# Performance work log

Hardware: AMD Instinct MI355X
Metric: run time of the kernel (lower is better)

## Reference

```python
import jax, jax.numpy as jnp
import numpy as np

N, NFEAT, NHID = 10000, 128, 64


def _gc(x, adj, W, b):
    # GraphConvolution: adj @ (x @ W) + b
    return adj @ (x @ W) + b


def _fwd(x, adj, Wg0, bg0, Wg1, bg1, Wt0, bt0, Wt1, bt1,
         W000, b000, W001, b001, W100, b100, W101, b101,
         Wo0, bo0, Wo1, bo1, Wpp, bpp, Wpp2, bpp2, a, t):
    H = Wg0.shape[1]
    # outcome GCN stack (n_in=2), dropout is eval no-op
    rep_o = jax.nn.relu(_gc(x, adj, Wg0, bg0))
    rep_o = jax.nn.relu(_gc(rep_o, adj, Wg1, bg1))
    # treatment GCN stack
    rep_t = jax.nn.relu(_gc(x, adj, Wt0, bt0))
    rep_t = jax.nn.relu(_gc(rep_t, adj, Wt1, bt1))

    rep_cat = jnp.concatenate([rep_o, rep_t], axis=1)  # [N, 2H]
    # edge score(i,j) = [rep_cat_i ; rep_cat_j] @ a  =  s_src_i + s_dst_j
    s_src = rep_cat @ a[:2 * H, 0]   # [N]
    s_dst = rep_cat @ a[2 * H:, 0]   # [N]
    scores = s_src[:, None] + s_dst[None, :]          # [N, N]
    # only nonzero adj entries get a score; rest remain 0 (index_put into zeros)
    att = jnp.where(adj != 0, scores, jnp.zeros((), scores.dtype))
    att = jax.nn.softmax(att, axis=1)                 # full dense row softmax

    rep_out = att @ rep_t + rep_o                     # [N, H]

    treatment = jax.nn.sigmoid((rep_t @ Wpp + bpp) @ Wpp2 + bpp2)  # [N, 2]

    rep0 = rep_out
    rep1 = rep_out
    y00 = jax.nn.relu(rep0 @ W000 + b000)
    y10 = jax.nn.relu(rep1 @ W100 + b100)
    y00 = jax.nn.relu(y00 @ W001 + b001)
    y10 = jax.nn.relu(y10 @ W101 + b101)
    y0 = (y00 @ Wo0 + bo0).reshape(-1)
    y1 = (y10 @ Wo1 + bo1).reshape(-1)
    y = jnp.where(t > 0, y1, y0)
    return (y, rep_out, treatment)


def setup_inputs() -> dict:
    key = jax.random.key(0)
    ks = jax.random.split(key, 32)
    H = NHID
    x = jax.random.normal(ks[0], (N, NFEAT), dtype=jnp.float32)
    u = jax.random.uniform(ks[1], (N, N), dtype=jnp.float32)
    adj = jnp.where(u < 0.002, u, jnp.zeros((), jnp.float32))
    t = jax.random.randint(ks[2], (N,), 0, 2, dtype=jnp.int32)

    def lin(k, fi, fo):
        s = 1.0 / np.sqrt(fi)
        kw, kb = jax.random.split(k)
        return (jax.random.uniform(kw, (fi, fo), jnp.float32, -s, s),
                jax.random.uniform(kb, (fo,), jnp.float32, -s, s))

    Wg0, bg0 = lin(ks[3], NFEAT, H)
    Wg1, bg1 = lin(ks[4], H, H)
    Wt0, bt0 = lin(ks[5], NFEAT, H)
    Wt1, bt1 = lin(ks[6], H, H)
    W000, b000 = lin(ks[7], H, H)
    W001, b001 = lin(ks[8], H, H)
    W100, b100 = lin(ks[9], H, H)
    W101, b101 = lin(ks[10], H, H)
    Wo0, bo0 = lin(ks[11], H, 1)
    Wo1, bo1 = lin(ks[12], H, 1)
    Wpp, bpp = lin(ks[13], H, H)
    Wpp2, bpp2 = lin(ks[14], H, 2)
    # torch init is xavier with gain=0 (all zeros); use small random for a
    # meaningful correctness baseline
    a = jax.random.normal(ks[15], (4 * H, 1), dtype=jnp.float32) * 0.1
    return dict(x=x, adj=adj, t=t,
                Wg0=Wg0, bg0=bg0, Wg1=Wg1, bg1=bg1,
                Wt0=Wt0, bt0=bt0, Wt1=Wt1, bt1=bt1,
                W000=W000, b000=b000, W001=W001, b001=b001,
                W100=W100, b100=b100, W101=W101, b101=b101,
                Wo0=Wo0, bo0=bo0, Wo1=Wo1, bo1=bo1,
                Wpp=Wpp, bpp=bpp, Wpp2=Wpp2, bpp2=bpp2, a=a)


def reference(x, adj, t, Wg0, bg0, Wg1, bg1, Wt0, bt0, Wt1, bt1,
              W000, b000, W001, b001, W100, b100, W101, b101,
              Wo0, bo0, Wo1, bo1, Wpp, bpp, Wpp2, bpp2, a):
    return _fwd(x, adj, Wg0, bg0, Wg1, bg1, Wt0, bt0, Wt1, bt1,
                W000, b000, W001, b001, W100, b100, W101, b101,
                Wo0, bo0, Wo1, bo1, Wpp, bpp, Wpp2, bpp2, a, t)
```

## Files before the change

### kernel.cpp

```cpp
#include <hip/hip_runtime.h>
#include <hip/hip_bf16.h>

#define N_NODES 10000
#define ROW4    2500
#define CAP     64
#define GEMM_BLOCKS 1250

#define OFF_CNT     0
#define OFF_COLSUM  10000
#define OFF_COLS    10064
#define OFF_VALS    650064
#define OFF_SSRC    1290064
#define OFF_SDST    1300064
#define OFF_B1      1310064
#define OFF_B2      1950064
#define OFF_B3      2590064
#define OFF_B4      3230064

__device__ __forceinline__ float wave_sum(float v) {
    #pragma unroll
    for (int off = 32; off >= 1; off >>= 1) v += __shfl_xor(v, off, 64);
    return v;
}
__device__ __forceinline__ float wave_max(float v) {
    #pragma unroll
    for (int off = 32; off >= 1; off >>= 1) v = fmaxf(v, __shfl_xor(v, off, 64));
    return v;
}

__global__ void k1_fused(const float4* __restrict__ adj4, const float* __restrict__ x,
                         const float* __restrict__ Wg0, const float* __restrict__ Wt0,
                         int* __restrict__ cnt, int* __restrict__ cols,
                         float* __restrict__ vals, float* __restrict__ colsum,
                         float* __restrict__ P, float* __restrict__ Q) {
    __shared__ float xs[8 * 128];
    int tid = threadIdx.x;
    if (blockIdx.x < GEMM_BLOCKS) {
        int row0 = blockIdx.x * 8;
        ((float4*)xs)[tid] = ((const float4*)(x + (size_t)row0 * 128))[tid];
        if (blockIdx.x == 0 && tid < 64) colsum[tid] = 0.0f;
        __syncthreads();
        int sub = tid >> 6, f = tid & 63;
        #pragma unroll
        for (int g = 0; g < 2; ++g) {
            const float* xr = xs + (g * 4 + sub) * 128;
            float aP = 0.0f, aQ = 0.0f;
            #pragma unroll 8
            for (int k = 0; k < 128; k += 4) {
                float4 xv = *(const float4*)(xr + k);
                aP += xv.x * Wg0[(k + 0) * 64 + f] + xv.y * Wg0[(k + 1) * 64 + f]
                    + xv.z * Wg0[(k + 2) * 64 + f] + xv.w * Wg0[(k + 3) * 64 + f];
                aQ += xv.x * Wt0[(k + 0) * 64 + f] + xv.y * Wt0[(k + 1) * 64 + f]
                    + xv.z * Wt0[(k + 2) * 64 + f] + xv.w * Wt0[(k + 3) * 64 + f];
            }
            P[(size_t)(row0 + g * 4 + sub) * 64 + f] = aP;
            Q[(size_t)(row0 + g * 4 + sub) * 64 + f] = aQ;
        }
    } else {
        int lane = tid & 63, w = tid >> 6;
        int row = (blockIdx.x - GEMM_BLOCKS) * 4 + w;
        const float4* rp = adj4 + (size_t)row * ROW4;
        size_t base = (size_t)row * CAP;
        int count = 0;
        for (int it = 0; it < 40; ++it) {
            int idx = it * 64 + lane;
            float4 v = make_float4(0.f, 0.f, 0.f, 0.f);
            if (idx < ROW4) v = rp[idx];
            float vv[4] = {v.x, v.y, v.z, v.w};
            bool any = (v.x != 0.f) | (v.y != 0.f) | (v.z != 0.f) | (v.w != 0.f);
            if (__ballot(any)) {
                #pragma unroll
                for (int l = 0; l < 4; ++l) {
                    unsigned long long b = __ballot(vv[l] != 0.f);
                    if (b) {
                        int pre = __popcll(b & ((1ull << lane) - 1ull));
                        if (vv[l] != 0.f) {
                            int pos = count + pre;
                            if (pos < CAP) {
                                cols[base + pos] = idx * 4 + l;
                                vals[base + pos] = vv[l];
                            }
                        }
                        count += (int)__popcll(b);
                    }
                }
            }
        }
        if (lane == 0) cnt[row] = min(count, CAP);
    }
}

__global__ void k2_agg_gemm(const int* __restrict__ cnt, const int* __restrict__ cols,
                            const float* __restrict__ vals,
                            const float* __restrict__ P, const float* __restrict__ Q,
                            const float* __restrict__ bg0, const float* __restrict__ bt0,
                            const float* __restrict__ Wg1, const float* __restrict__ Wt1,
                            float* __restrict__ P2, float* __restrict__ Q2) {
    __shared__ float ra[8 * 64], rb[8 * 64];
    int tid = threadIdx.x, row0 = blockIdx.x * 8, sub = tid >> 6, f = tid & 63;
    float bo = bg0[f], bt = bt0[f];
    #pragma unroll
    for (int g = 0; g < 2; ++g) {
        int lr = g * 4 + sub, row = row0 + lr;
        int c = min(cnt[row], CAP);
        float v_l = 0.0f; int c_l = 0;
        if (f < c) { c_l = cols[(size_t)row * CAP + f]; v_l = vals[(size_t)row * CAP + f]; }
        float a0 = 0.f, a1 = 0.f, b0 = 0.f, b1 = 0.f;
        for (int p = 0; p < c; p += 8) {
            #pragma unroll
            for (int j = 0; j < 8; j += 2) {
                float vv0 = __shfl(v_l, p + j, 64);     int cc0 = __shfl(c_l, p + j, 64);
                float vv1 = __shfl(v_l, p + j + 1, 64); int cc1 = __shfl(c_l, p + j + 1, 64);
                a0 += vv0 * P[(size_t)cc0 * 64 + f];
                b0 += vv0 * Q[(size_t)cc0 * 64 + f];
                a1 += vv1 * P[(size_t)cc1 * 64 + f];
                b1 += vv1 * Q[(size_t)cc1 * 64 + f];
            }
        }
        ra[lr * 64 + f] = fmaxf(a0 + a1 + bo, 0.0f);
        rb[lr * 64 + f] = fmaxf(b0 + b1 + bt, 0.0f);
    }
    __syncthreads();
    #pragma unroll
    for (int g = 0; g < 2; ++g) {
        int lr = g * 4 + sub, row = row0 + lr;
        const float* rra = ra + lr * 64;
        const float* rrb = rb + lr * 64;
        float aA = 0.f, aB = 0.f;
        #pragma unroll 8
        for (int k = 0; k < 64; k += 4) {
            float4 va = *(const float4*)(rra + k);
            float4 vb = *(const float4*)(rrb + k);
            aA += va.x * Wg1[(k + 0) * 64 + f] + va.y * Wg1[(k + 1) * 64 + f]
                + va.z * Wg1[(k + 2) * 64 + f] + va.w * Wg1[(k + 3) * 64 + f];
            aB += vb.x * Wt1[(k + 0) * 64 + f] + vb.y * Wt1[(k + 1) * 64 + f]
                + vb.z * Wt1[(k + 2) * 64 + f] + vb.w * Wt1[(k + 3) * 64 + f];
        }
        P2[(size_t)row * 64 + f] = aA;
        Q2[(size_t)row * 64 + f] = aB;
    }
}

__global__ void k3_agg_score(const int* __restrict__ cnt, const int* __restrict__ cols,
                             const float* __restrict__ vals,
                             const float* __restrict__ P2, const float* __restrict__ Q2,
                             const float* __restrict__ bg1, const float* __restrict__ bt1,
                             const float* __restrict__ a,
                             const float* __restrict__ Wpp, const float* __restrict__ bpp,
                             const float* __restrict__ Wpp2, const float* __restrict__ bpp2,
                             float* __restrict__ rep_o, float* __restrict__ rep_t,
                             float* __restrict__ s_src, float* __restrict__ s_dst,
                             float* __restrict__ colsum, float* __restrict__ out_trt) {
    __shared__ float rts[8 * 64];
    int tid = threadIdx.x, row0 = blockIdx.x * 8, sub = tid >> 6, f = tid & 63;
    float bo = bg1[f], bt = bt1[f];
    float a0c = a[f], a1c = a[64 + f], a2c = a[128 + f], a3c = a[192 + f];
    #pragma unroll
    for (int g = 0; g < 2; ++g) {
        int lr = g * 4 + sub, row = row0 + lr;
        int c = min(cnt[row], CAP);
        float v_l = 0.0f; int c_l = 0;
        if (f < c) { c_l = cols[(size_t)row * CAP + f]; v_l = vals[(size_t)row * CAP + f]; }
        float a0 = 0.f, a1 = 0.f, b0 = 0.f, b1 = 0.f;
        for (int p = 0; p < c; p += 8) {
            #pragma unroll
            for (int j = 0; j < 8; j += 2) {
                float vv0 = __shfl(v_l, p + j, 64);     int cc0 = __shfl(c_l, p + j, 64);
                float vv1 = __shfl(v_l, p + j + 1, 64); int cc1 = __shfl(c_l, p + j + 1, 64);
                a0 += vv0 * P2[(size_t)cc0 * 64 + f];
                b0 += vv0 * Q2[(size_t)cc0 * 64 + f];
                a1 += vv1 * P2[(size_t)cc1 * 64 + f];
                b1 += vv1 * Q2[(size_t)cc1 * 64 + f];
            }
        }
        float vo = fmaxf(a0 + a1 + bo, 0.0f);
        float vt = fmaxf(b0 + b1 + bt, 0.0f);
        rep_o[(size_t)row * 64 + f] = vo;
        rep_t[(size_t)row * 64 + f] = vt;
        rts[lr * 64 + f] = vt;
        float ps = wave_sum(vo * a0c + vt * a1c);
        float pd = wave_sum(vo * a2c + vt * a3c);
        if (f == 0) { s_src[row] = ps; s_dst[row] = pd; }
    }
    __syncthreads();
    if (sub == 0) {
        float cs = 0.0f;
        #pragma unroll
        for (int lr = 0; lr < 8; ++lr) cs += rts[lr * 64 + f];
        atomicAdd(&colsum[f], cs);
    }
    float bp = bpp[f], w20 = Wpp2[f * 2 + 0], w21 = Wpp2[f * 2 + 1];
    #pragma unroll
    for (int g = 0; g < 2; ++g) {
        int lr = g * 4 + sub, row = row0 + lr;
        const float* rr = rts + lr * 64;
        float u = bp;
        #pragma unroll 8
        for (int k = 0; k < 64; k += 4) {
            float4 rv = *(const float4*)(rr + k);
            u += rv.x * Wpp[(k + 0) * 64 + f] + rv.y * Wpp[(k + 1) * 64 + f]
               + rv.z * Wpp[(k + 2) * 64 + f] + rv.w * Wpp[(k + 3) * 64 + f];
        }
        float p0 = wave_sum(u * w20);
        float p1 = wave_sum(u * w21);
        if (f == 0) {
            out_trt[(size_t)row * 2 + 0] = 1.0f / (1.0f + expf(-(p0 + bpp2[0])));
            out_trt[(size_t)row * 2 + 1] = 1.0f / (1.0f + expf(-(p1 + bpp2[1])));
        }
    }
}

__global__ void k4_attn_heads(const int* __restrict__ cnt, const int* __restrict__ cols,
                              const float* __restrict__ s_src, const float* __restrict__ s_dst,
                              const float* __restrict__ colsum,
                              const float* __restrict__ rep_o, const float* __restrict__ rep_t,
                              const float* __restrict__ W000, const float* __restrict__ b000,
                              const float* __restrict__ W001, const float* __restrict__ b001,
                              const float* __restrict__ W100, const float* __restrict__ b100,
                              const float* __restrict__ W101, const float* __restrict__ b101,
                              const float* __restrict__ Wo0, const float* __restrict__ bo0,
                              const float* __restrict__ Wo1, const float* __restrict__ bo1,
                              const int* __restrict__ t,
                              float* __restrict__ out_y, float* __restrict__ out_rep) {
    __shared__ float reps[8 * 64], u0s[8 * 64], u1s[8 * 64];
    int tid = threadIdx.x, row0 = blockIdx.x * 8, sub = tid >> 6, f = tid & 63;
    float csf = colsum[f];
    #pragma unroll
    for (int g = 0; g < 2; ++g) {
        int lr = g * 4 + sub, row = row0 + lr;
        int c = min(cnt[row], CAP);
        float ssrc = s_src[row];
        int   col_l = (f < c) ? cols[(size_t)row * CAP + f] : 0;
        float s_l   = (f < c) ? ssrc + s_dst[col_l] : -1e30f;
        float m = fmaxf(wave_max(s_l), 0.0f);
        float e_l = (f < c) ? expf(s_l - m) : 0.0f;
        float em = expf(-m);
        float Z = wave_sum(e_l) + (float)(N_NODES - c) * em;
        float g_l = (f < c) ? (e_l - em) : 0.0f;
        float a0 = 0.f, a1 = 0.f, a2 = 0.f, a3 = 0.f;
        for (int p = 0; p < c; p += 8) {
            #pragma unroll
            for (int j = 0; j < 8; j += 4) {
                float g0 = __shfl(g_l, p + j + 0, 64); int c0 = __shfl(col_l, p + j + 0, 64);
                float g1 = __shfl(g_l, p + j + 1, 64); int c1 = __shfl(col_l, p + j + 1, 64);
                float g2 = __shfl(g_l, p + j + 2, 64); int c2 = __shfl(col_l, p + j + 2, 64);
                float g3 = __shfl(g_l, p + j + 3, 64); int c3 = __shfl(col_l, p + j + 3, 64);
                a0 += g0 * rep_t[(size_t)c0 * 64 + f];
                a1 += g1 * rep_t[(size_t)c1 * 64 + f];
                a2 += g2 * rep_t[(size_t)c2 * 64 + f];
                a3 += g3 * rep_t[(size_t)c3 * 64 + f];
            }
        }
        float outv = ((a0 + a1 + a2 + a3) + em * csf) / Z + rep_o[(size_t)row * 64 + f];
        out_rep[(size_t)row * 64 + f] = outv;
        reps[lr * 64 + f] = outv;
    }
    __syncthreads();
    float bA = b000[f], bB = b100[f];
    #pragma unroll
    for (int g = 0; g < 2; ++g) {
        int lr = g * 4 + sub;
        const float* rr = reps + lr * 64;
        float u0 = bA, u1 = bB;
        #pragma unroll 8
        for (int k = 0; k < 64; k += 4) {
            float4 rv = *(const float4*)(rr + k);
            u0 += rv.x * W000[(k + 0) * 64 + f] + rv.y * W000[(k + 1) * 64 + f]
                + rv.z * W000[(k + 2) * 64 + f] + rv.w * W000[(k + 3) * 64 + f];
            u1 += rv.x * W100[(k + 0) * 64 + f] + rv.y * W100[(k + 1) * 64 + f]
                + rv.z * W100[(k + 2) * 64 + f] + rv.w * W100[(k + 3) * 64 + f];
        }
        u0s[lr * 64 + f] = fmaxf(u0, 0.0f);
        u1s[lr * 64 + f] = fmaxf(u1, 0.0f);
    }
    __syncthreads();
    float bC = b001[f], bD = b101[f], wo0 = Wo0[f], wo1 = Wo1[f];
    #pragma unroll
    for (int g = 0; g < 2; ++g) {
        int lr = g * 4 + sub, row = row0 + lr;
        const float* r0 = u0s + lr * 64;
        const float* r1 = u1s + lr * 64;
        float v0 = bC, v1 = bD;
        #pragma unroll 8
        for (int k = 0; k < 64; k += 4) {
            float4 q0 = *(const float4*)(r0 + k);
            float4 q1 = *(const float4*)(r1 + k);
            v0 += q0.x * W001[(k + 0) * 64 + f] + q0.y * W001[(k + 1) * 64 + f]
                + q0.z * W001[(k + 2) * 64 + f] + q0.w * W001[(k + 3) * 64 + f];
            v1 += q1.x * W101[(k + 0) * 64 + f] + q1.y * W101[(k + 1) * 64 + f]
                + q1.z * W101[(k + 2) * 64 + f] + q1.w * W101[(k + 3) * 64 + f];
        }
        float y0 = wave_sum(fmaxf(v0, 0.0f) * wo0);
        float y1 = wave_sum(fmaxf(v1, 0.0f) * wo1);
        if (f == 0)
            out_y[row] = (t[row] > 0) ? (y1 + bo1[0]) : (y0 + bo0[0]);
    }
}


extern "C" void kernel_launch(void* const* d_in, const int* in_sizes, int n_in,
                              void* d_out, int out_size, void* d_ws, size_t ws_size,
                              hipStream_t stream) {
    const float* x    = (const float*)d_in[0];
    const float* adj  = (const float*)d_in[1];
    const int*   t    = (const int*)d_in[2];
    const float* Wg0  = (const float*)d_in[3];
    const float* bg0  = (const float*)d_in[4];
    const float* Wg1  = (const float*)d_in[5];
    const float* bg1  = (const float*)d_in[6];
    const float* Wt0  = (const float*)d_in[7];
    const float* bt0  = (const float*)d_in[8];
    const float* Wt1  = (const float*)d_in[9];
    const float* bt1  = (const float*)d_in[10];
    const float* W000 = (const float*)d_in[11];
    const float* b000 = (const float*)d_in[12];
    const float* W001 = (const float*)d_in[13];
    const float* b001 = (const float*)d_in[14];
    const float* W100 = (const float*)d_in[15];
    const float* b100 = (const float*)d_in[16];
    const float* W101 = (const float*)d_in[17];
    const float* b101 = (const float*)d_in[18];
    const float* Wo0  = (const float*)d_in[19];
    const float* bo0  = (const float*)d_in[20];
    const float* Wo1  = (const float*)d_in[21];
    const float* bo1  = (const float*)d_in[22];
    const float* Wpp  = (const float*)d_in[23];
    const float* bpp  = (const float*)d_in[24];
    const float* Wpp2 = (const float*)d_in[25];
    const float* bpp2 = (const float*)d_in[26];
    const float* a    = (const float*)d_in[27];

    float* ws = (float*)d_ws;
    int*   cnt    = (int*)(ws + OFF_CNT);
    float* colsum = ws + OFF_COLSUM;
    int*   cols   = (int*)(ws + OFF_COLS);
    float* vals   = ws + OFF_VALS;
    float* s_src  = ws + OFF_SSRC;
    float* s_dst  = ws + OFF_SDST;
    float* B1     = ws + OFF_B1;
    float* B2     = ws + OFF_B2;
    float* B3     = ws + OFF_B3;
    float* B4     = ws + OFF_B4;

    float* out_y   = (float*)d_out;
    float* out_rep = (float*)d_out + N_NODES;
    float* out_trt = (float*)d_out + N_NODES + N_NODES * 64;

    k1_fused<<<GEMM_BLOCKS + 2500, 256, 0, stream>>>((const float4*)adj, x, Wg0, Wt0,
                                                     cnt, cols, vals, colsum, B1, B2);
    k2_agg_gemm<<<1250, 256, 0, stream>>>(cnt, cols, vals, B1, B2, bg0, bt0, Wg1, Wt1, B3, B4);
    k3_agg_score<<<1250, 256, 0, stream>>>(cnt, cols, vals, B3, B4, bg1, bt1, a,
                                           Wpp, bpp, Wpp2, bpp2,
                                           B1, B2, s_src, s_dst, colsum, out_trt);
    k4_attn_heads<<<1250, 256, 0, stream>>>(cnt, cols, s_src, s_dst, colsum, B1, B2,
                                            W000, b000, W001, b001,
                                            W100, b100, W101, b101,
                                            Wo0, bo0, Wo1, bo1, t, out_y, out_rep);
}
```

Baseline: 690.4 us.

## Merge four kernels into one cooperative persistent kernel with grid syncs

Replaces the four separate kernel launches with a single cooperative persistent kernel whose blocks loop over row chunks and separate the phases with grid-wide syncs. It also packs column indices and values into interleaved float2 pairs so each neighbour needs one load instead of two. The aim is to cut launch overhead and the gaps between dependent kernels. In exchange it caps the grid size, adds grid-sync cost, and calls an occupancy query on the host for every launch.

```diff
diff --git a/kernel.cpp b/kernel.cpp
--- a/kernel.cpp
+++ b/kernel.cpp
@@ -1,17 +1,22 @@
 #include <hip/hip_runtime.h>
-#include <hip/hip_bf16.h>
+#include <hip/hip_cooperative_groups.h>
+
+namespace cg = cooperative_groups;
 
 #define N_NODES 10000
 #define ROW4    2500
 #define CAP     64
-#define GEMM_BLOCKS 1250
+#define GEMM_CHUNKS 1250
+#define SPAR_CHUNKS 2500
+#define TOTAL_A     (GEMM_CHUNKS + SPAR_CHUNKS)
+#define ROW_CHUNKS  1250
+#define MAX_GRID    1024
 
 #define OFF_CNT     0
 #define OFF_COLSUM  10000
-#define OFF_COLS    10064
-#define OFF_VALS    650064
-#define OFF_SSRC    1290064
-#define OFF_SDST    1300064
+#define OFF_SSRC    10064
+#define OFF_SDST    20064
+#define OFF_PAIRS   30064
 #define OFF_B1      1310064
 #define OFF_B2      1950064
 #define OFF_B3      2590064
@@ -28,332 +33,315 @@
     return v;
 }
 
-__global__ void k1_fused(const float4* __restrict__ adj4, const float* __restrict__ x,
-                         const float* __restrict__ Wg0, const float* __restrict__ Wt0,
-                         int* __restrict__ cnt, int* __restrict__ cols,
-                         float* __restrict__ vals, float* __restrict__ colsum,
-                         float* __restrict__ P, float* __restrict__ Q) {
-    __shared__ float xs[8 * 128];
-    int tid = threadIdx.x;
-    if (blockIdx.x < GEMM_BLOCKS) {
-        int row0 = blockIdx.x * 8;
-        ((float4*)xs)[tid] = ((const float4*)(x + (size_t)row0 * 128))[tid];
-        if (blockIdx.x == 0 && tid < 64) colsum[tid] = 0.0f;
-        __syncthreads();
-        int sub = tid >> 6, f = tid & 63;
-        #pragma unroll
-        for (int g = 0; g < 2; ++g) {
-            const float* xr = xs + (g * 4 + sub) * 128;
-            float aP = 0.0f, aQ = 0.0f;
-            #pragma unroll 8
-            for (int k = 0; k < 128; k += 4) {
-                float4 xv = *(const float4*)(xr + k);
-                aP += xv.x * Wg0[(k + 0) * 64 + f] + xv.y * Wg0[(k + 1) * 64 + f]
-                    + xv.z * Wg0[(k + 2) * 64 + f] + xv.w * Wg0[(k + 3) * 64 + f];
-                aQ += xv.x * Wt0[(k + 0) * 64 + f] + xv.y * Wt0[(k + 1) * 64 + f]
-                    + xv.z * Wt0[(k + 2) * 64 + f] + xv.w * Wt0[(k + 3) * 64 + f];
-            }
-            P[(size_t)(row0 + g * 4 + sub) * 64 + f] = aP;
-            Q[(size_t)(row0 + g * 4 + sub) * 64 + f] = aQ;
+struct KArgs {
+    const float4* adj4; const float* x; const int* t;
+    const float *Wg0, *bg0, *Wg1, *bg1, *Wt0, *bt0, *Wt1, *bt1;
+    const float *W000, *b000, *W001, *b001, *W100, *b100, *W101, *b101;
+    const float *Wo0, *bo0, *Wo1, *bo1, *Wpp, *bpp, *Wpp2, *bpp2, *a;
+    int* cnt; float2* pairs;
+    float *colsum, *s_src, *s_dst, *B1, *B2, *B3, *B4;
+    float *out_y, *out_rep, *out_trt;
+};
+
+__global__ __launch_bounds__(256, 4) void mega(KArgs A) {
+    __shared__ float smem[1536];
+    const int tid = threadIdx.x;
+    const int sub = tid >> 6, f = tid & 63;
+    cg::grid_group grid = cg::this_grid();
+
+    if (blockIdx.x == 0 && tid < 64) A.colsum[tid] = 0.0f;
+    for (int chunk = blockIdx.x; chunk < TOTAL_A; chunk += gridDim.x) {
+        if (chunk < GEMM_CHUNKS) {
+            int row0 = chunk * 8;
+            float* xs = smem;
+            ((float4*)xs)[tid] = ((const float4*)(A.x + (size_t)row0 * 128))[tid];
+            __syncthreads();
+            #pragma unroll
+            for (int g = 0; g < 2; ++g) {
+                const float* xr = xs + (g * 4 + sub) * 128;
+                float aP = 0.0f, aQ = 0.0f;
+                #pragma unroll 8
+                for (int k = 0; k < 128; k += 4) {
+                    float4 xv = *(const float4*)(xr + k);
+                    aP += xv.x * A.Wg0[(k + 0) * 64 + f] + xv.y * A.Wg0[(k + 1) * 64 + f]
+                        + xv.z * A.Wg0[(k + 2) * 64 + f] + xv.w * A.Wg0[(k + 3) * 64 + f];
+                    aQ += xv.x * A.Wt0[(k + 0) * 64 + f] + xv.y * A.Wt0[(k + 1) * 64 + f]
+                        + xv.z * A.Wt0[(k + 2) * 64 + f] + xv.w * A.Wt0[(k + 3) * 64 + f];
+                }
+                A.B1[(size_t)(row0 + g * 4 + sub) * 64 + f] = aP;
+                A.B2[(size_t)(row0 + g * 4 + sub) * 64 + f] = aQ;
+            }
+            __syncthreads();
+        } else {
+            int row = (chunk - GEMM_CHUNKS) * 4 + sub;
+            const float4* rp = A.adj4 + (size_t)row * ROW4;
+            size_t base = (size_t)row * CAP;
+            int count = 0;
+            for (int it = 0; it < 40; ++it) {
+                int idx = it * 64 + f;
+                float4 v = make_float4(0.f, 0.f, 0.f, 0.f);
+                if (idx < ROW4) v = rp[idx];
+                float vv[4] = {v.x, v.y, v.z, v.w};
+                bool any = (v.x != 0.f) | (v.y != 0.f) | (v.z != 0.f) | (v.w != 0.f);
+                if (__ballot(any)) {
+                    #pragma unroll
+                    for (int l = 0; l < 4; ++l) {
+                        unsigned long long b = __ballot(vv[l] != 0.f);
+                        if (b) {
+                            int pre = __popcll(b & ((1ull << f) - 1ull));
+                            if (vv[l] != 0.f) {
+                                int pos = count + pre;
+                                if (pos < CAP)
+                                    A.pairs[base + pos] =
+                                        make_float2(__int_as_float(idx * 4 + l), vv[l]);
+                            }
+                            count += (int)__popcll(b);
+                        }
+                    }
+                }
+            }
+            if (f == 0) A.cnt[row] = min(count, CAP);
         }
-    } else {
-        int lane = tid & 63, w = tid >> 6;
-        int row = (blockIdx.x - GEMM_BLOCKS) * 4 + w;
-        const float4* rp = adj4 + (size_t)row * ROW4;
-        size_t base = (size_t)row * CAP;
-        int count = 0;
-        for (int it = 0; it < 40; ++it) {
-            int idx = it * 64 + lane;
-            float4 v = make_float4(0.f, 0.f, 0.f, 0.f);
-            if (idx < ROW4) v = rp[idx];
-            float vv[4] = {v.x, v.y, v.z, v.w};
-            bool any = (v.x != 0.f) | (v.y != 0.f) | (v.z != 0.f) | (v.w != 0.f);
-            if (__ballot(any)) {
+    }
+    grid.sync();
+
+    {
+        float* ra = smem; float* rb = smem + 512;
+        float bo = A.bg0[f], bt = A.bt0[f];
+        for (int chunk = blockIdx.x; chunk < ROW_CHUNKS; chunk += gridDim.x) {
+            int row0 = chunk * 8;
+            #pragma unroll
+            for (int g = 0; g < 2; ++g) {
+                int lr = g * 4 + sub, row = row0 + lr;
+                int c = min(A.cnt[row], CAP);
+                float2 pr = make_float2(0.f, 0.f);
+                if (f < c) pr = A.pairs[(size_t)row * CAP + f];
+                int c_l = __float_as_int(pr.x); float v_l = pr.y;
+                float a0 = 0.f, a1 = 0.f, b0 = 0.f, b1 = 0.f;
+                for (int p = 0; p < c; p += 8) {
+                    #pragma unroll
+                    for (int j = 0; j < 8; j += 2) {
+                        float vv0 = __shfl(v_l, p + j, 64);     int cc0 = __shfl(c_l, p + j, 64);
+                        float vv1 = __shfl(v_l, p + j + 1, 64); int cc1 = __shfl(c_l, p + j + 1, 64);
+                        a0 += vv0 * A.B1[(size_t)cc0 * 64 + f];
+                        b0 += vv0 * A.B2[(size_t)cc0 * 64 + f];
+                        a1 += vv1 * A.B1[(size_t)cc1 * 64 + f];
+                        b1 += vv1 * A.B2[(size_t)cc1 * 64 + f];
+                    }
+                }
+                ra[lr * 64 + f] = fmaxf(a0 + a1 + bo, 0.0f);
+                rb[lr * 64 + f] = fmaxf(b0 + b1 + bt, 0.0f);
+            }
+            __syncthreads();
+            #pragma unroll
+            for (int g = 0; g < 2; ++g) {
+                int lr = g * 4 + sub, row = row0 + lr;
+                const float* rra = ra + lr * 64;
+                const float* rrb = rb + lr * 64;
+                float aA = 0.f, aB = 0.f;
+                #pragma unroll 8
+                for (int k = 0; k < 64; k += 4) {
+                    float4 va = *(const float4*)(rra + k);
+                    float4 vb = *(const float4*)(rrb + k);
+                    aA += va.x * A.Wg1[(k + 0) * 64 + f] + va.y * A.Wg1[(k + 1) * 64 + f]
+                        + va.z * A.Wg1[(k + 2) * 64 + f] + va.w * A.Wg1[(k + 3) * 64 + f];
+                    aB += vb.x * A.Wt1[(k + 0) * 64 + f] + vb.y * A.Wt1[(k + 1) * 64 + f]
+                        + vb.z * A.Wt1[(k + 2) * 64 + f] + vb.w * A.Wt1[(k + 3) * 64 + f];
+                }
+                A.B3[(size_t)row * 64 + f] = aA;
+                A.B4[(size_t)row * 64 + f] = aB;
+            }
+            __syncthreads();
+        }
+    }
+    grid.sync();
+
+    {
+        float* rts = smem;
+        float bo = A.bg1[f], bt = A.bt1[f];
+        float a0c = A.a[f], a1c = A.a[64 + f], a2c = A.a[128 + f], a3c = A.a[192 + f];
+        float bp = A.bpp[f], w20 = A.Wpp2[f * 2 + 0], w21 = A.Wpp2[f * 2 + 1];
+        for (int chunk = blockIdx.x; chunk < ROW_CHUNKS; chunk += gridDim.x) {
+            int row0 = chunk * 8;
+            #pragma unroll
+            for (int g = 0; g < 2; ++g) {
+                int lr = g * 4 + sub, row = row0 + lr;
+                int c = min(A.cnt[row], CAP);
+                float2 pr = make_float2(0.f, 0.f);
+                if (f < c) pr = A.pairs[(size_t)row * CAP + f];
+                int c_l = __float_as_int(pr.x); float v_l = pr.y;
+                float a0 = 0.f, a1 = 0.f, b0 = 0.f, b1 = 0.f;
+                for (int p = 0; p < c; p += 8) {
+                    #pragma unroll
+                    for (int j = 0; j < 8; j += 2) {
+                        float vv0 = __shfl(v_l, p + j, 64);     int cc0 = __shfl(c_l, p + j, 64);
+                        float vv1 = __shfl(v_l, p + j + 1, 64); int cc1 = __shfl(c_l, p + j + 1, 64);
+                        a0 += vv0 * A.B3[(size_t)cc0 * 64 + f];
+                        b0 += vv0 * A.B4[(size_t)cc0 * 64 + f];
+                        a1 += vv1 * A.B3[(size_t)cc1 * 64 + f];
+                        b1 += vv1 * A.B4[(size_t)cc1 * 64 + f];
+                    }
+                }
+                float vo = fmaxf(a0 + a1 + bo, 0.0f);
+                float vt = fmaxf(b0 + b1 + bt, 0.0f);
+                A.B1[(size_t)row * 64 + f] = vo;
+                A.B2[(size_t)row * 64 + f] = vt;
+                rts[lr * 64 + f] = vt;
+                float ps = wave_sum(vo * a0c + vt * a1c);
+                float pd = wave_sum(vo * a2c + vt * a3c);
+                if (f == 0) { A.s_src[row] = ps; A.s_dst[row] = pd; }
+            }
+            __syncthreads();
+            if (sub == 0) {
+                float cs = 0.0f;
                 #pragma unroll
-                for (int l = 0; l < 4; ++l) {
-                    unsigned long long b = __ballot(vv[l] != 0.f);
-                    if (b) {
-                        int pre = __popcll(b & ((1ull << lane) - 1ull));
-                        if (vv[l] != 0.f) {
-                            int pos = count + pre;
-                            if (pos < CAP) {
-                                cols[base + pos] = idx * 4 + l;
-                                vals[base + pos] = vv[l];
-                            }
-                        }
-                        count += (int)__popcll(b);
+                for (int lr = 0; lr < 8; ++lr) cs += rts[lr * 64 + f];
+                atomicAdd(&A.colsum[f], cs);
+            }
+            #pragma unroll
+            for (int g = 0; g < 2; ++g) {
+                int lr = g * 4 + sub, row = row0 + lr;
+                const float* rr = rts + lr * 64;
+                float u = bp;
+                #pragma unroll 8
+                for (int k = 0; k < 64; k += 4) {
+                    float4 rv = *(const float4*)(rr + k);
+                    u += rv.x * A.Wpp[(k + 0) * 64 + f] + rv.y * A.Wpp[(k + 1) * 64 + f]
+                       + rv.z * A.Wpp[(k + 2) * 64 + f] + rv.w * A.Wpp[(k + 3) * 64 + f];
+                }
+                float p0 = wave_sum(u * w20);
+                float p1 = wave_sum(u * w21);
+                if (f == 0) {
+                    A.out_trt[(size_t)row * 2 + 0] = 1.0f / (1.0f + expf(-(p0 + A.bpp2[0])));
+                    A.out_trt[(size_t)row * 2 + 1] = 1.0f / (1.0f + expf(-(p1 + A.bpp2[1])));
+                }
+            }
+            __syncthreads();
+        }
+    }
+    grid.sync();
+
+    {
+        float* reps = smem; float* u0s = smem + 512; float* u1s = smem + 1024;
+        float csf = A.colsum[f];
+        float bA = A.b000[f], bB = A.b100[f];
+        float bC = A.b001[f], bD = A.b101[f], wo0 = A.Wo0[f], wo1 = A.Wo1[f];
+        for (int chunk = blockIdx.x; chunk < ROW_CHUNKS; chunk += gridDim.x) {
+            int row0 = chunk * 8;
+            #pragma unroll
+            for (int g = 0; g < 2; ++g) {
+                int lr = g * 4 + sub, row = row0 + lr;
+                int c = min(A.cnt[row], CAP);
+                float ssrc = A.s_src[row];
+                int   col_l = (f < c) ? __float_as_int(A.pairs[(size_t)row * CAP + f].x) : 0;
+                float s_l   = (f < c) ? ssrc + A.s_dst[col_l] : -1e30f;
+                float m = fmaxf(wave_max(s_l), 0.0f);
+                float e_l = (f < c) ? expf(s_l - m) : 0.0f;
+                float em = expf(-m);
+                float Z = wave_sum(e_l) + (float)(N_NODES - c) * em;
+                float g_l = (f < c) ? (e_l - em) : 0.0f;
+                float a0 = 0.f, a1 = 0.f, a2 = 0.f, a3 = 0.f;
+                for (int p = 0; p < c; p += 8) {
+                    #pragma unroll
+                    for (int j = 0; j < 8; j += 4) {
+                        float g0 = __shfl(g_l, p + j + 0, 64); int c0 = __shfl(col_l, p + j + 0, 64);
+                        float g1 = __shfl(g_l, p + j + 1, 64); int c1 = __shfl(col_l, p + j + 1, 64);
+                        float g2 = __shfl(g_l, p + j + 2, 64); int c2 = __shfl(col_l, p + j + 2, 64);
+                        float g3 = __shfl(g_l, p + j + 3, 64); int c3 = __shfl(col_l, p + j + 3, 64);
+                        a0 += g0 * A.B2[(size_t)c0 * 64 + f];
+                        a1 += g1 * A.B2[(size_t)c1 * 64 + f];
+                        a2 += g2 * A.B2[(size_t)c2 * 64 + f];
+                        a3 += g3 * A.B2[(size_t)c3 * 64 + f];
                     }
                 }
-            }
-        }
-        if (lane == 0) cnt[row] = min(count, CAP);
-    }
-}
-
-__global__ void k2_agg_gemm(const int* __restrict__ cnt, const int* __restrict__ cols,
-                            const float* __restrict__ vals,
-                            const float* __restrict__ P, const float* __restrict__ Q,
-                            const float* __restrict__ bg0, const float* __restrict__ bt0,
-                            const float* __restrict__ Wg1, const float* __restrict__ Wt1,
-                            float* __restrict__ P2, float* __restrict__ Q2) {
-    __shared__ float ra[8 * 64], rb[8 * 64];
-    int tid = threadIdx.x, row0 = blockIdx.x * 8, sub = tid >> 6, f = tid & 63;
-    float bo = bg0[f], bt = bt0[f];
-    #pragma unroll
-    for (int g = 0; g < 2; ++g) {
-        int lr = g * 4 + sub, row = row0 + lr;
-        int c = min(cnt[row], CAP);
-        float v_l = 0.0f; int c_l = 0;
-        if (f < c) { c_l = cols[(size_t)row * CAP + f]; v_l = vals[(size_t)row * CAP + f]; }
-        float a0 = 0.f, a1 = 0.f, b0 = 0.f, b1 = 0.f;
-        for (int p = 0; p < c; p += 8) {
-            #pragma unroll
-            for (int j = 0; j < 8; j += 2) {
-                float vv0 = __shfl(v_l, p + j, 64);     int cc0 = __shfl(c_l, p + j, 64);
-                float vv1 = __shfl(v_l, p + j + 1, 64); int cc1 = __shfl(c_l, p + j + 1, 64);
-                a0 += vv0 * P[(size_t)cc0 * 64 + f];
-                b0 += vv0 * Q[(size_t)cc0 * 64 + f];
-                a1 += vv1 * P[(size_t)cc1 * 64 + f];
-                b1 += vv1 * Q[(size_t)cc1 * 64 + f];
-            }
-        }
-        ra[lr * 64 + f] = fmaxf(a0 + a1 + bo, 0.0f);
-        rb[lr * 64 + f] = fmaxf(b0 + b1 + bt, 0.0f);
-    }
-    __syncthreads();
-    #pragma unroll
-    for (int g = 0; g < 2; ++g) {
-        int lr = g * 4 + sub, row = row0 + lr;
-        const float* rra = ra + lr * 64;
-        const float* rrb = rb + lr * 64;
-        float aA = 0.f, aB = 0.f;
-        #pragma unroll 8
-        for (int k = 0; k < 64; k += 4) {
-            float4 va = *(const float4*)(rra + k);
-            float4 vb = *(const float4*)(rrb + k);
-            aA += va.x * Wg1[(k + 0) * 64 + f] + va.y * Wg1[(k + 1) * 64 + f]
-                + va.z * Wg1[(k + 2) * 64 + f] + va.w * Wg1[(k + 3) * 64 + f];
-            aB += vb.x * Wt1[(k + 0) * 64 + f] + vb.y * Wt1[(k + 1) * 64 + f]
-                + vb.z * Wt1[(k + 2) * 64 + f] + vb.w * Wt1[(k + 3) * 64 + f];
-        }
-        P2[(size_t)row * 64 + f] = aA;
-        Q2[(size_t)row * 64 + f] = aB;
-    }
-}
-
-__global__ void k3_agg_score(const int* __restrict__ cnt, const int* __restrict__ cols,
-                             const float* __restrict__ vals,
-                             const float* __restrict__ P2, const float* __restrict__ Q2,
-                             const float* __restrict__ bg1, const float* __restrict__ bt1,
-                             const float* __restrict__ a,
-                             const float* __restrict__ Wpp, const float* __restrict__ bpp,
-                             const float* __restrict__ Wpp2, const float* __restrict__ bpp2,
-                             float* __restrict__ rep_o, float* __restrict__ rep_t,
-                             float* __restrict__ s_src, float* __restrict__ s_dst,
-                             float* __restrict__ colsum, float* __restrict__ out_trt) {
-    __shared__ float rts[8 * 64];
-    int tid = threadIdx.x, row0 = blockIdx.x * 8, sub = tid >> 6, f = tid & 63;
-    float bo = bg1[f], bt = bt1[f];
-    float a0c = a[f], a1c = a[64 + f], a2c = a[128 + f], a3c = a[192 + f];
-    #pragma unroll
-    for (int g = 0; g < 2; ++g) {
-        int lr = g * 4 + sub, row = row0 + lr;
-        int c = min(cnt[row], CAP);
-        float v_l = 0.0f; int c_l = 0;
-        if (f < c) { c_l = cols[(size_t)row * CAP + f]; v_l = vals[(size_t)row * CAP + f]; }
-        float a0 = 0.f, a1 = 0.f, b0 = 0.f, b1 = 0.f;
-        for (int p = 0; p < c; p += 8) {
-            #pragma unroll
-            for (int j = 0; j < 8; j += 2) {
-                float vv0 = __shfl(v_l, p + j, 64);     int cc0 = __shfl(c_l, p + j, 64);
-                float vv1 = __shfl(v_l, p + j + 1, 64); int cc1 = __shfl(c_l, p + j + 1, 64);
-                a0 += vv0 * P2[(size_t)cc0 * 64 + f];
-                b0 += vv0 * Q2[(size_t)cc0 * 64 + f];
-                a1 += vv1 * P2[(size_t)cc1 * 64 + f];
-                b1 += vv1 * Q2[(size_t)cc1 * 64 + f];
-            }
-        }
-        float vo = fmaxf(a0 + a1 + bo, 0.0f);
-        float vt = fmaxf(b0 + b1 + bt, 0.0f);
-        rep_o[(size_t)row * 64 + f] = vo;
-        rep_t[(size_t)row * 64 + f] = vt;
-        rts[lr * 64 + f] = vt;
-        float ps = wave_sum(vo * a0c + vt * a1c);
-        float pd = wave_sum(vo * a2c + vt * a3c);
-        if (f == 0) { s_src[row] = ps; s_dst[row] = pd; }
-    }
-    __syncthreads();
-    if (sub == 0) {
-        float cs = 0.0f;
-        #pragma unroll
-        for (int lr = 0; lr < 8; ++lr) cs += rts[lr * 64 + f];
-        atomicAdd(&colsum[f], cs);
-    }
-    float bp = bpp[f], w20 = Wpp2[f * 2 + 0], w21 = Wpp2[f * 2 + 1];
-    #pragma unroll
-    for (int g = 0; g < 2; ++g) {
-        int lr = g * 4 + sub, row = row0 + lr;
-        const float* rr = rts + lr * 64;
-        float u = bp;
-        #pragma unroll 8
-        for (int k = 0; k < 64; k += 4) {
-            float4 rv = *(const float4*)(rr + k);
-            u += rv.x * Wpp[(k + 0) * 64 + f] + rv.y * Wpp[(k + 1) * 64 + f]
-               + rv.z * Wpp[(k + 2) * 64 + f] + rv.w * Wpp[(k + 3) * 64 + f];
-        }
-        float p0 = wave_sum(u * w20);
-        float p1 = wave_sum(u * w21);
-        if (f == 0) {
-            out_trt[(size_t)row * 2 + 0] = 1.0f / (1.0f + expf(-(p0 + bpp2[0])));
-            out_trt[(size_t)row * 2 + 1] = 1.0f / (1.0f + expf(-(p1 + bpp2[1])));
+                float outv = ((a0 + a1 + a2 + a3) + em * csf) / Z + A.B1[(size_t)row * 64 + f];
+                A.out_rep[(size_t)row * 64 + f] = outv;
+                reps[lr * 64 + f] = outv;
+            }
+            __syncthreads();
+            #pragma unroll
+            for (int g = 0; g < 2; ++g) {
+                int lr = g * 4 + sub;
+                const float* rr = reps + lr * 64;
+                float u0 = bA, u1 = bB;
+                #pragma unroll 8
+                for (int k = 0; k < 64; k += 4) {
+                    float4 rv = *(const float4*)(rr + k);
+                    u0 += rv.x * A.W000[(k + 0) * 64 + f] + rv.y * A.W000[(k + 1) * 64 + f]
+                        + rv.z * A.W000[(k + 2) * 64 + f] + rv.w * A.W000[(k + 3) * 64 + f];
+                    u1 += rv.x * A.W100[(k + 0) * 64 + f] + rv.y * A.W100[(k + 1) * 64 + f]
+                        + rv.z * A.W100[(k + 2) * 64 + f] + rv.w * A.W100[(k + 3) * 64 + f];
+                }
+                u0s[lr * 64 + f] = fmaxf(u0, 0.0f);
+                u1s[lr * 64 + f] = fmaxf(u1, 0.0f);
+            }
+            __syncthreads();
+            #pragma unroll
+            for (int g = 0; g < 2; ++g) {
+                int lr = g * 4 + sub, row = row0 + lr;
+                const float* r0 = u0s + lr * 64;
+                const float* r1 = u1s + lr * 64;
+                float v0 = bC, v1 = bD;
+                #pragma unroll 8
+                for (int k = 0; k < 64; k += 4) {
+                    float4 q0 = *(const float4*)(r0 + k);
+                    float4 q1 = *(const float4*)(r1 + k);
+                    v0 += q0.x * A.W001[(k + 0) * 64 + f] + q0.y * A.W001[(k + 1) * 64 + f]
+                        + q0.z * A.W001[(k + 2) * 64 + f] + q0.w * A.W001[(k + 3) * 64 + f];
+                    v1 += q1.x * A.W101[(k + 0) * 64 + f] + q1.y * A.W101[(k + 1) * 64 + f]
+                        + q1.z * A.W101[(k + 2) * 64 + f] + q1.w * A.W101[(k + 3) * 64 + f];
+                }
+                float y0 = wave_sum(fmaxf(v0, 0.0f) * wo0);
+                float y1 = wave_sum(fmaxf(v1, 0.0f) * wo1);
+                if (f == 0)
+                    A.out_y[row] = (A.t[row] > 0) ? (y1 + A.bo1[0]) : (y0 + A.bo0[0]);
+            }
+            __syncthreads();
         }
     }
 }
 
-__global__ void k4_attn_heads(const int* __restrict__ cnt, const int* __restrict__ cols,
-                              const float* __restrict__ s_src, const float* __restrict__ s_dst,
-                              const float* __restrict__ colsum,
-                              const float* __restrict__ rep_o, const float* __restrict__ rep_t,
-                              const float* __restrict__ W000, const float* __restrict__ b000,
-                              const float* __restrict__ W001, const float* __restrict__ b001,
-                              const float* __restrict__ W100, const float* __restrict__ b100,
-                              const float* __restrict__ W101, const float* __restrict__ b101,
-                              const float* __restrict__ Wo0, const float* __restrict__ bo0,
-                              const float* __restrict__ Wo1, const float* __restrict__ bo1,
-                              const int* __restrict__ t,
-                              float* __restrict__ out_y, float* __restrict__ out_rep) {
-    __shared__ float reps[8 * 64], u0s[8 * 64], u1s[8 * 64];
-    int tid = threadIdx.x, row0 = blockIdx.x * 8, sub = tid >> 6, f = tid & 63;
-    float csf = colsum[f];
-    #pragma unroll
-    for (int g = 0; g < 2; ++g) {
-        int lr = g * 4 + sub, row = row0 + lr;
-        int c = min(cnt[row], CAP);
-        float ssrc = s_src[row];
-        int   col_l = (f < c) ? cols[(size_t)row * CAP + f] : 0;
-        float s_l   = (f < c) ? ssrc + s_dst[col_l] : -1e30f;
-        float m = fmaxf(wave_max(s_l), 0.0f);
-        float e_l = (f < c) ? expf(s_l - m) : 0.0f;
-        float em = expf(-m);
-        float Z = wave_sum(e_l) + (float)(N_NODES - c) * em;
-        float g_l = (f < c) ? (e_l - em) : 0.0f;
-        float a0 = 0.f, a1 = 0.f, a2 = 0.f, a3 = 0.f;
-        for (int p = 0; p < c; p += 8) {
-            #pragma unroll
-            for (int j = 0; j < 8; j += 4) {
-                float g0 = __shfl(g_l, p + j + 0, 64); int c0 = __shfl(col_l, p + j + 0, 64);
-                float g1 = __shfl(g_l, p + j + 1, 64); int c1 = __shfl(col_l, p + j + 1, 64);
-                float g2 = __shfl(g_l, p + j + 2, 64); int c2 = __shfl(col_l, p + j + 2, 64);
-                float g3 = __shfl(g_l, p + j + 3, 64); int c3 = __shfl(col_l, p + j + 3, 64);
-                a0 += g0 * rep_t[(size_t)c0 * 64 + f];
-                a1 += g1 * rep_t[(size_t)c1 * 64 + f];
-                a2 += g2 * rep_t[(size_t)c2 * 64 + f];
-                a3 += g3 * rep_t[(size_t)c3 * 64 + f];
-            }
-        }
-        float outv = ((a0 + a1 + a2 + a3) + em * csf) / Z + rep_o[(size_t)row * 64 + f];
-        out_rep[(size_t)row * 64 + f] = outv;
-        reps[lr * 64 + f] = outv;
-    }
-    __syncthreads();
-    float bA = b000[f], bB = b100[f];
-    #pragma unroll
-    for (int g = 0; g < 2; ++g) {
-        int lr = g * 4 + sub;
-        const float* rr = reps + lr * 64;
-        float u0 = bA, u1 = bB;
-        #pragma unroll 8
-        for (int k = 0; k < 64; k += 4) {
-            float4 rv = *(const float4*)(rr + k);
-            u0 += rv.x * W000[(k + 0) * 64 + f] + rv.y * W000[(k + 1) * 64 + f]
-                + rv.z * W000[(k + 2) * 64 + f] + rv.w * W000[(k + 3) * 64 + f];
-            u1 += rv.x * W100[(k + 0) * 64 + f] + rv.y * W100[(k + 1) * 64 + f]
-                + rv.z * W100[(k + 2) * 64 + f] + rv.w * W100[(k + 3) * 64 + f];
-        }
-        u0s[lr * 64 + f] = fmaxf(u0, 0.0f);
-        u1s[lr * 64 + f] = fmaxf(u1, 0.0f);
-    }
-    __syncthreads();
-    float bC = b001[f], bD = b101[f], wo0 = Wo0[f], wo1 = Wo1[f];
-    #pragma unroll
-    for (int g = 0; g < 2; ++g) {
-        int lr = g * 4 + sub, row = row0 + lr;
-        const float* r0 = u0s + lr * 64;
-        const float* r1 = u1s + lr * 64;
-        float v0 = bC, v1 = bD;
-        #pragma unroll 8
-        for (int k = 0; k < 64; k += 4) {
-            float4 q0 = *(const float4*)(r0 + k);
-            float4 q1 = *(const float4*)(r1 + k);
-            v0 += q0.x * W001[(k + 0) * 64 + f] + q0.y * W001[(k + 1) * 64 + f]
-                + q0.z * W001[(k + 2) * 64 + f] + q0.w * W001[(k + 3) * 64 + f];
-            v1 += q1.x * W101[(k + 0) * 64 + f] + q1.y * W101[(k + 1) * 64 + f]
-                + q1.z * W101[(k + 2) * 64 + f] + q1.w * W101[(k + 3) * 64 + f];
-        }
-        float y0 = wave_sum(fmaxf(v0, 0.0f) * wo0);
-        float y1 = wave_sum(fmaxf(v1, 0.0f) * wo1);
-        if (f == 0)
-            out_y[row] = (t[row] > 0) ? (y1 + bo1[0]) : (y0 + bo0[0]);
-    }
-}
-
 
 extern "C" void kernel_launch(void* const* d_in, const int* in_sizes, int n_in,
                               void* d_out, int out_size, void* d_ws, size_t ws_size,
                               hipStream_t stream) {
-    const float* x    = (const float*)d_in[0];
-    const float* adj  = (const float*)d_in[1];
-    const int*   t    = (const int*)d_in[2];
-    const float* Wg0  = (const float*)d_in[3];
-    const float* bg0  = (const float*)d_in[4];
-    const float* Wg1  = (const float*)d_in[5];
-    const float* bg1  = (const float*)d_in[6];
-    const float* Wt0  = (const float*)d_in[7];
-    const float* bt0  = (const float*)d_in[8];
-    const float* Wt1  = (const float*)d_in[9];
-    const float* bt1  = (const float*)d_in[10];
-    const float* W000 = (const float*)d_in[11];
-    const float* b000 = (const float*)d_in[12];
-    const float* W001 = (const float*)d_in[13];
-    const float* b001 = (const float*)d_in[14];
-    const float* W100 = (const float*)d_in[15];
-    const float* b100 = (const float*)d_in[16];
-    const float* W101 = (const float*)d_in[17];
-    const float* b101 = (const float*)d_in[18];
-    const float* Wo0  = (const float*)d_in[19];
-    const float* bo0  = (const float*)d_in[20];
-    const float* Wo1  = (const float*)d_in[21];
-    const float* bo1  = (const float*)d_in[22];
-    const float* Wpp  = (const float*)d_in[23];
-    const float* bpp  = (const float*)d_in[24];
-    const float* Wpp2 = (const float*)d_in[25];
-    const float* bpp2 = (const float*)d_in[26];
-    const float* a    = (const float*)d_in[27];
-
     float* ws = (float*)d_ws;
-    int*   cnt    = (int*)(ws + OFF_CNT);
-    float* colsum = ws + OFF_COLSUM;
-    int*   cols   = (int*)(ws + OFF_COLS);
-    float* vals   = ws + OFF_VALS;
-    float* s_src  = ws + OFF_SSRC;
-    float* s_dst  = ws + OFF_SDST;
-    float* B1     = ws + OFF_B1;
-    float* B2     = ws + OFF_B2;
-    float* B3     = ws + OFF_B3;
-    float* B4     = ws + OFF_B4;
-
-    float* out_y   = (float*)d_out;
-    float* out_rep = (float*)d_out + N_NODES;
-    float* out_trt = (float*)d_out + N_NODES + N_NODES * 64;
-
-    k1_fused<<<GEMM_BLOCKS + 2500, 256, 0, stream>>>((const float4*)adj, x, Wg0, Wt0,
-                                                     cnt, cols, vals, colsum, B1, B2);
-    k2_agg_gemm<<<1250, 256, 0, stream>>>(cnt, cols, vals, B1, B2, bg0, bt0, Wg1, Wt1, B3, B4);
-    k3_agg_score<<<1250, 256, 0, stream>>>(cnt, cols, vals, B3, B4, bg1, bt1, a,
-                                           Wpp, bpp, Wpp2, bpp2,
-                                           B1, B2, s_src, s_dst, colsum, out_trt);
-    k4_attn_heads<<<1250, 256, 0, stream>>>(cnt, cols, s_src, s_dst, colsum, B1, B2,
-                                            W000, b000, W001, b001,
-                                            W100, b100, W101, b101,
-                                            Wo0, bo0, Wo1, bo1, t, out_y, out_rep);
+    KArgs ka;
+    ka.x    = (const float*)d_in[0];
+    ka.adj4 = (const float4*)d_in[1];
+    ka.t    = (const int*)d_in[2];
+    ka.Wg0  = (const float*)d_in[3];  ka.bg0  = (const float*)d_in[4];
+    ka.Wg1  = (const float*)d_in[5];  ka.bg1  = (const float*)d_in[6];
+    ka.Wt0  = (const float*)d_in[7];  ka.bt0  = (const float*)d_in[8];
+    ka.Wt1  = (const float*)d_in[9];  ka.bt1  = (const float*)d_in[10];
+    ka.W000 = (const float*)d_in[11]; ka.b000 = (const float*)d_in[12];
+    ka.W001 = (const float*)d_in[13]; ka.b001 = (const float*)d_in[14];
+    ka.W100 = (const float*)d_in[15]; ka.b100 = (const float*)d_in[16];
+    ka.W101 = (const float*)d_in[17]; ka.b101 = (const float*)d_in[18];
+    ka.Wo0  = (const float*)d_in[19]; ka.bo0  = (const float*)d_in[20];
+    ka.Wo1  = (const float*)d_in[21]; ka.bo1  = (const float*)d_in[22];
+    ka.Wpp  = (const float*)d_in[23]; ka.bpp  = (const float*)d_in[24];
+    ka.Wpp2 = (const float*)d_in[25]; ka.bpp2 = (const float*)d_in[26];
+    ka.a    = (const float*)d_in[27];
+    ka.cnt    = (int*)(ws + OFF_CNT);
+    ka.colsum = ws + OFF_COLSUM;
+    ka.s_src  = ws + OFF_SSRC;
+    ka.s_dst  = ws + OFF_SDST;
+    ka.pairs  = (float2*)(ws + OFF_PAIRS);
+    ka.B1     = ws + OFF_B1;
+    ka.B2     = ws + OFF_B2;
+    ka.B3     = ws + OFF_B3;
+    ka.B4     = ws + OFF_B4;
+    ka.out_y   = (float*)d_out;
+    ka.out_rep = (float*)d_out + N_NODES;
+    ka.out_trt = (float*)d_out + N_NODES + N_NODES * 64;
+
+    int nb = 0;
+    hipOccupancyMaxActiveBlocksPerMultiprocessor(&nb, (const void*)mega, 256, 0);
+    if (nb <= 0) nb = 4;
+    int grid = nb * 256;
+    if (grid > MAX_GRID) grid = MAX_GRID;
+
+    void* kp[] = { (void*)&ka };
+    hipLaunchCooperativeKernel((const void*)mega, dim3(grid), dim3(256), kp, 0, stream);
 }
```

Measured after the change: 973.4 us. 41.0% more time.
